# Performance work log

Hardware: AMD Instinct MI355X
Metric: run time of the kernel (lower is better)

## Reference

```python
import jax, jax.numpy as jnp
import numpy as np
import math

B, N, F = 4, 4096, 64
NEG_SLOPE = 0.01


def _leaky_relu(x):
    return jnp.where(x >= 0, x, NEG_SLOPE * x)


def setup_inputs() -> dict:
    key = jax.random.key(0)
    k1, k2, k3, k4, k5 = jax.random.split(key, 5)
    Q = jax.random.normal(k1, (B, N, F, 2), dtype=jnp.float32)
    K = jax.random.normal(k2, (B, N, F, 2), dtype=jnp.float32)
    V = jax.random.normal(k3, (B, N, F, 2), dtype=jnp.float32)
    W_att = jax.random.normal(k4, (F, F), dtype=jnp.float32) / math.sqrt(F)
    b_att = jax.random.normal(k5, (F,), dtype=jnp.float32) * 0.01
    return {"Q": Q, "K": K, "V": V, "W_att": W_att, "b_att": b_att}


def reference(Q, K, V, W_att, b_att):
    # Split complex components: last axis is (real, imag)
    Qr, Qi = Q[..., 0], Q[..., 1]
    Kr, Ki = K[..., 0], K[..., 1]
    Vr, Vi = V[..., 0], V[..., 1]

    n = Q.shape[1]
    scale = 1.0 / math.sqrt(n)  # num_nodes == N

    # Complex scores = Q @ K^T (no conjugation, as in torch einsum on complex)
    sr = (jnp.einsum('bik,bjk->bij', Qr, Kr) - jnp.einsum('bik,bjk->bij', Qi, Ki)) * scale
    si = (jnp.einsum('bik,bjk->bij', Qr, Ki) + jnp.einsum('bik,bjk->bij', Qi, Kr)) * scale

    # Causal mask: positions j > i are masked out (contribute zero weight)
    causal = jnp.tril(jnp.ones((n, n), dtype=bool))  # [N, N], True = keep
    wr = jnp.where(causal, _leaky_relu(sr), 0.0)
    wi = jnp.where(causal, _leaky_relu(si), 0.0)

    # Attention-weighted values (real weights with real V, imag with imag V)
    out_r = jnp.einsum('bij,bjf->bif', wr, Vr)
    out_i = jnp.einsum('bij,bjf->bif', wi, Vi)

    # att_map: shared linear layer
    out_r = out_r @ W_att.T + b_att
    out_i = out_i @ W_att.T + b_att

    return jnp.stack([out_r, out_i], axis=-1)  # [B, N, F, 2]
```

## Files before the change

### kernel.cpp

```cpp
#include <hip/hip_runtime.h>

#define NB 4
#define NN 4096
#define NF 64
#define TSTEP 8
#define BLKS_PER_B 260

typedef __attribute__((ext_vector_type(8))) short bf16x8;
typedef __attribute__((ext_vector_type(4))) float f32x4;

union S8 { unsigned short u[8]; bf16x8 v; };

__device__ __forceinline__ unsigned short f2bf(float x) {
    unsigned int uu = __builtin_bit_cast(unsigned int, x);
    uu += 0x7fffu + ((uu >> 16) & 1u);
    return (unsigned short)(uu >> 16);
}

__global__ __launch_bounds__(256)
void prep_all(const float* __restrict__ Q, const float* __restrict__ K,
              const float* __restrict__ V, const float* __restrict__ W,
              const float* __restrict__ batt,
              short* __restrict__ QF, short* __restrict__ KF,
              short* __restrict__ VF, short* __restrict__ WF,
              float* __restrict__ out) {
    int tid = blockIdx.x * 256 + threadIdx.x;

    if (tid < 262144) {
        int sel = tid >> 17;
        int r   = tid & 0x1FFFF;
        int l  = r & 63;
        int c  = (r >> 6) & 1;
        int rg = (r >> 7) & 255;
        int b  = r >> 15;
        const float* src = sel ? K : Q;
        short*       dst = sel ? KF : QF;
        float sc = sel ? 1.0f : 0.015625f;

        int row = rg * 16 + (l & 15);
        int k0  = c * 32 + (l >> 4) * 8;
        const float4* s4 = (const float4*)src;
        int base4 = (b * NN + row) * 32 + (k0 >> 1);

        S8 ar, ai;
        #pragma unroll
        for (int m = 0; m < 4; ++m) {
            float4 f = s4[base4 + m];
            ar.u[2 * m]     = f2bf(f.x * sc);
            ar.u[2 * m + 1] = f2bf(f.z * sc);
            ai.u[2 * m]     = f2bf(f.y * sc);
            ai.u[2 * m + 1] = f2bf(f.w * sc);
        }
        int cid0 = ((b * 256 + rg) * 2 + c) * 2;
        *(bf16x8*)(dst + (cid0 + 0) * 512 + l * 8) = ar.v;
        *(bf16x8*)(dst + (cid0 + 1) * 512 + l * 8) = ai.v;
    } else if (tid < 393216) {
        int r = tid - 262144;
        int l  = r & 63;
        int c  = (r >> 6) & 1;
        int ft = (r >> 7) & 3;
        int jt = (r >> 9) & 63;
        int b  = (r >> 15) & 3;

        int f  = ft * 16 + (l & 15);
        int jb = jt * 64 + c * 32 + (l >> 4) * 4;
        const float2* s2 = (const float2*)V;

        S8 ar, ai;
        #pragma unroll
        for (int e = 0; e < 8; ++e) {
            int j = jb + (e >> 2) * 16 + (e & 3);
            float2 gg = s2[(b * NN + j) * 64 + f];
            ar.u[e] = f2bf(gg.x);
            ai.u[e] = f2bf(gg.y);
        }
        int cid0 = (((b * 64 + jt) * 4 + ft) * 2 + c) * 2;
        *(bf16x8*)(VF + (cid0 + 0) * 512 + l * 8) = ar.v;
        *(bf16x8*)(VF + (cid0 + 1) * 512 + l * 8) = ai.v;
    } else if (tid < 393728) {
        int r = tid - 393216;
        int l  = r & 63;
        int c  = (r >> 6) & 1;
        int gt = r >> 7;
        int grow = gt * 16 + (l & 15);
        const float* sp = W + grow * 64;
        S8 a;
        #pragma unroll
        for (int e = 0; e < 8; ++e) {
            int f = c * 32 + (e >> 2) * 16 + (l >> 4) * 4 + (e & 3);
            a.u[e] = f2bf(sp[f]);
        }
        *(bf16x8*)(WF + ((gt * 2 + c) * 64 + l) * 8) = a.v;
    } else {
        int r = tid - 393728;
        int g0 = (2 * r) & 63;
        float b0 = batt[g0];
        float b1 = batt[g0 + 1];
        float4 zz = {b0, b0, b1, b1};
        ((float4*)out)[r] = zz;
    }
}

__device__ __forceinline__ int tri_inv(int g) {
    int it = (int)((__builtin_sqrtf(8.0f * (float)g + 1.0f) - 1.0f) * 0.5f);
    while ((it + 1) * (it + 2) / 2 <= g) ++it;
    while (it * (it + 1) / 2 > g) --it;
    return it;
}

__global__ __launch_bounds__(256, 4)
void attn_main(const short* __restrict__ QF, const short* __restrict__ KF,
               const short* __restrict__ VF, const short* __restrict__ WF,
               const float* __restrict__ batt, float* __restrict__ out) {
    int bid = blockIdx.x;
    int b   = bid / BLKS_PER_B;
    int g   = (bid % BLKS_PER_B) * TSTEP;
    int gend = g + TSTEP;

    int w   = threadIdx.x >> 6;
    int l   = threadIdx.x & 63;
    int r16 = l & 15;
    int lb  = l >> 4;

    const f32x4 z = {0.f, 0.f, 0.f, 0.f};

    while (g < gend) {
        int it   = tri_inv(g);
        int base = it * (it + 1) / 2;
        int jt0  = g - base;
        int cnt  = min(gend - g, it + 1 - jt0);
        int jt1  = jt0 + cnt;

        bf16x8 qf[2][2];
        {
            int rgq = it * 4 + w;
            #pragma unroll
            for (int c = 0; c < 2; ++c)
                #pragma unroll
                for (int ch = 0; ch < 2; ++ch)
                    qf[c][ch] = *(const bf16x8*)(QF + (((b * 256 + rgq) * 2 + c) * 2 + ch) * 512 + l * 8);
        }

        f32x4 o[4][2];
        #pragma unroll
        for (int ft = 0; ft < 4; ++ft) { o[ft][0] = z; o[ft][1] = z; }

        for (int jt = jt0; jt < jt1; ++jt) {
            bool diag = (jt == it);
            bf16x8 pa0r, pa0i, pa1r, pa1i;

            #pragma unroll
            for (int ct = 0; ct < 4; ++ct) {
                bf16x8 kf[2][2];
                int rg = jt * 4 + ct;
                #pragma unroll
                for (int c = 0; c < 2; ++c)
                    #pragma unroll
                    for (int ch = 0; ch < 2; ++ch)
                        kf[c][ch] = *(const bf16x8*)(KF + (((b * 256 + rg) * 2 + c) * 2 + ch) * 512 + l * 8);

                f32x4 t1 = __builtin_amdgcn_mfma_f32_16x16x32_bf16(kf[0][0], qf[0][0], z, 0, 0, 0);
                t1 = __builtin_amdgcn_mfma_f32_16x16x32_bf16(kf[1][0], qf[1][0], t1, 0, 0, 0);
                f32x4 t2 = __builtin_amdgcn_mfma_f32_16x16x32_bf16(kf[0][1], qf[0][1], z, 0, 0, 0);
                t2 = __builtin_amdgcn_mfma_f32_16x16x32_bf16(kf[1][1], qf[1][1], t2, 0, 0, 0);
                f32x4 si = __builtin_amdgcn_mfma_f32_16x16x32_bf16(kf[0][1], qf[0][0], z, 0, 0, 0);
                si = __builtin_amdgcn_mfma_f32_16x16x32_bf16(kf[1][1], qf[1][0], si, 0, 0, 0);
                si = __builtin_amdgcn_mfma_f32_16x16x32_bf16(kf[0][0], qf[0][1], si, 0, 0, 0);
                si = __builtin_amdgcn_mfma_f32_16x16x32_bf16(kf[1][0], qf[1][1], si, 0, 0, 0);

                #pragma unroll
                for (int reg = 0; reg < 4; ++reg) {
                    float sr = t1[reg] - t2[reg];
                    float sv = si[reg];
                    float wr = fmaxf(sr, 0.f) + 0.01f * fminf(sr, 0.f);
                    float wi = fmaxf(sv, 0.f) + 0.01f * fminf(sv, 0.f);
                    if (diag) {
                        int jg = ct * 16 + lb * 4 + reg;
                        int ig = w * 16 + r16;
                        if (jg > ig) { wr = 0.f; wi = 0.f; }
                    }
                    short hr = (short)f2bf(wr);
                    short hi = (short)f2bf(wi);
                    int e = (ct & 1) * 4 + reg;
                    if (ct < 2) { pa0r[e] = hr; pa0i[e] = hi; }
                    else        { pa1r[e] = hr; pa1i[e] = hi; }
                }
            }

            #pragma unroll
            for (int ft = 0; ft < 4; ++ft) {
                int cid0 = (((b * 64 + jt) * 4 + ft) * 2 + 0) * 2;
                bf16x8 v0r = *(const bf16x8*)(VF + (cid0 + 0) * 512 + l * 8);
                bf16x8 v0i = *(const bf16x8*)(VF + (cid0 + 1) * 512 + l * 8);
                bf16x8 v1r = *(const bf16x8*)(VF + (cid0 + 2) * 512 + l * 8);
                bf16x8 v1i = *(const bf16x8*)(VF + (cid0 + 3) * 512 + l * 8);
                o[ft][0] = __builtin_amdgcn_mfma_f32_16x16x32_bf16(v0r, pa0r, o[ft][0], 0, 0, 0);
                o[ft][0] = __builtin_amdgcn_mfma_f32_16x16x32_bf16(v1r, pa1r, o[ft][0], 0, 0, 0);
                o[ft][1] = __builtin_amdgcn_mfma_f32_16x16x32_bf16(v0i, pa0i, o[ft][1], 0, 0, 0);
                o[ft][1] = __builtin_amdgcn_mfma_f32_16x16x32_bf16(v1i, pa1i, o[ft][1], 0, 0, 0);
            }
        }

        bf16x8 ob[2][2];
        #pragma unroll
        for (int cc = 0; cc < 2; ++cc)
            #pragma unroll
            for (int ch = 0; ch < 2; ++ch)
                #pragma unroll
                for (int s = 0; s < 2; ++s)
                    #pragma unroll
                    for (int reg = 0; reg < 4; ++reg)
                        ob[cc][ch][s * 4 + reg] = (short)f2bf(o[cc * 2 + s][ch][reg]);

        bool whole = (jt0 == 0) && (jt1 == it + 1);
        int i0 = it * 64 + w * 16;

        #pragma unroll
        for (int gt = 0; gt < 4; ++gt) {
            bf16x8 wa0 = *(const bf16x8*)(WF + ((gt * 2 + 0) * 64 + l) * 8);
            bf16x8 wa1 = *(const bf16x8*)(WF + ((gt * 2 + 1) * 64 + l) * 8);

            f32x4 a0 = __builtin_amdgcn_mfma_f32_16x16x32_bf16(ob[0][0], wa0, z, 0, 0, 0);
            a0 = __builtin_amdgcn_mfma_f32_16x16x32_bf16(ob[1][0], wa1, a0, 0, 0, 0);
            f32x4 a1 = __builtin_amdgcn_mfma_f32_16x16x32_bf16(ob[0][1], wa0, z, 0, 0, 0);
            a1 = __builtin_amdgcn_mfma_f32_16x16x32_bf16(ob[1][1], wa1, a1, 0, 0, 0);

            int gcol = gt * 16 + r16;
            if (whole) {
                float bb = batt[gcol];
                #pragma unroll
                for (int reg = 0; reg < 4; ++reg) {
                    int irow = i0 + lb * 4 + reg;
                    float2 st = {a0[reg] + bb, a1[reg] + bb};
                    *(float2*)(out + ((b * NN + irow) * 64 + gcol) * 2) = st;
                }
            } else {
                #pragma unroll
                for (int reg = 0; reg < 4; ++reg) {
                    int irow = i0 + lb * 4 + reg;
                    int idx = ((b * NN + irow) * 64 + gcol) * 2;
                    atomicAdd(out + idx,     a0[reg]);
                    atomicAdd(out + idx + 1, a1[reg]);
                }
            }
        }

        g += cnt;
    }
}

extern "C" void kernel_launch(void* const* d_in, const int* in_sizes, int n_in,
                              void* d_out, int out_size, void* d_ws, size_t ws_size,
                              hipStream_t stream) {
    const float* Q  = (const float*)d_in[0];
    const float* K  = (const float*)d_in[1];
    const float* V  = (const float*)d_in[2];
    const float* W  = (const float*)d_in[3];
    const float* bA = (const float*)d_in[4];
    float* out = (float*)d_out;

    short* QF = (short*)d_ws;
    short* KF = QF + 2097152;
    short* VF = KF + 2097152;
    short* WF = VF + 2097152;

    prep_all<<<3586, 256, 0, stream>>>(Q, K, V, W, bA, QF, KF, VF, WF, out);
    attn_main<<<NB * BLKS_PER_B, 256, 0, stream>>>(QF, KF, VF, WF, bA, out);
}
```

Baseline: 185.7 us.

## Stage K/V tiles in shared memory and specialize diagonal tile compute

Before this change each of the four waves loaded the full K and V tiles from global memory on its own. Now the block cooperatively loads them once per key tile into a 32 KB LDS buffer, with a barrier before and after, so global/L2 traffic drops about fourfold. The diagonal-mask branch becomes a template parameter so off-diagonal tiles skip the mask check. The hand-written bf16 rounding and leaky-relu are swapped for library and select-based forms. The costs are two barriers per tile with no double buffering, so load latency is no longer overlapped, and more LDS use that may limit occupancy.

```diff
diff --git a/kernel.cpp b/kernel.cpp
--- a/kernel.cpp
+++ b/kernel.cpp
@@ -1,4 +1,5 @@
 #include <hip/hip_runtime.h>
+#include <hip/hip_bf16.h>
 
 #define NB 4
 #define NN 4096
@@ -15,6 +16,10 @@
     unsigned int uu = __builtin_bit_cast(unsigned int, x);
     uu += 0x7fffu + ((uu >> 16) & 1u);
     return (unsigned short)(uu >> 16);
+}
+
+__device__ __forceinline__ short f2bf_s(float x) {
+    return __builtin_bit_cast(short, __float2bfloat16(x));
 }
 
 __global__ __launch_bounds__(256)
@@ -108,10 +113,70 @@
     return it;
 }
 
+template<bool DIAG>
+__device__ __forceinline__ void tile_compute(const short* sb, int w, int l,
+                                             int r16, int lb,
+                                             const bf16x8 (&qf)[2][2],
+                                             f32x4 (&o)[4][2]) {
+    const f32x4 z = {0.f, 0.f, 0.f, 0.f};
+    bf16x8 pa0r, pa0i, pa1r, pa1i;
+
+    #pragma unroll
+    for (int ct = 0; ct < 4; ++ct) {
+        const short* kb = sb + (ct * 4) * 512 + l * 8;
+        bf16x8 kf00 = *(const bf16x8*)(kb);
+        bf16x8 kf01 = *(const bf16x8*)(kb + 512);
+        bf16x8 kf10 = *(const bf16x8*)(kb + 1024);
+        bf16x8 kf11 = *(const bf16x8*)(kb + 1536);
+
+        f32x4 t1 = __builtin_amdgcn_mfma_f32_16x16x32_bf16(kf00, qf[0][0], z, 0, 0, 0);
+        t1 = __builtin_amdgcn_mfma_f32_16x16x32_bf16(kf10, qf[1][0], t1, 0, 0, 0);
+        f32x4 t2 = __builtin_amdgcn_mfma_f32_16x16x32_bf16(kf01, qf[0][1], z, 0, 0, 0);
+        t2 = __builtin_amdgcn_mfma_f32_16x16x32_bf16(kf11, qf[1][1], t2, 0, 0, 0);
+        f32x4 si = __builtin_amdgcn_mfma_f32_16x16x32_bf16(kf01, qf[0][0], z, 0, 0, 0);
+        si = __builtin_amdgcn_mfma_f32_16x16x32_bf16(kf11, qf[1][0], si, 0, 0, 0);
+        si = __builtin_amdgcn_mfma_f32_16x16x32_bf16(kf00, qf[0][1], si, 0, 0, 0);
+        si = __builtin_amdgcn_mfma_f32_16x16x32_bf16(kf10, qf[1][1], si, 0, 0, 0);
+
+        #pragma unroll
+        for (int reg = 0; reg < 4; ++reg) {
+            float sr = t1[reg] - t2[reg];
+            float sv = si[reg];
+            float wr = sr * (sr >= 0.f ? 1.0f : 0.01f);
+            float wi = sv * (sv >= 0.f ? 1.0f : 0.01f);
+            if constexpr (DIAG) {
+                int jg = ct * 16 + lb * 4 + reg;
+                int ig = w * 16 + r16;
+                if (jg > ig) { wr = 0.f; wi = 0.f; }
+            }
+            short hr = f2bf_s(wr);
+            short hi = f2bf_s(wi);
+            int e = (ct & 1) * 4 + reg;
+            if (ct < 2) { pa0r[e] = hr; pa0i[e] = hi; }
+            else        { pa1r[e] = hr; pa1i[e] = hi; }
+        }
+    }
+
+    #pragma unroll
+    for (int ft = 0; ft < 4; ++ft) {
+        const short* vb = sb + (16 + ft * 4) * 512 + l * 8;
+        bf16x8 v0r = *(const bf16x8*)(vb);
+        bf16x8 v0i = *(const bf16x8*)(vb + 512);
+        bf16x8 v1r = *(const bf16x8*)(vb + 1024);
+        bf16x8 v1i = *(const bf16x8*)(vb + 1536);
+        o[ft][0] = __builtin_amdgcn_mfma_f32_16x16x32_bf16(v0r, pa0r, o[ft][0], 0, 0, 0);
+        o[ft][0] = __builtin_amdgcn_mfma_f32_16x16x32_bf16(v1r, pa1r, o[ft][0], 0, 0, 0);
+        o[ft][1] = __builtin_amdgcn_mfma_f32_16x16x32_bf16(v0i, pa0i, o[ft][1], 0, 0, 0);
+        o[ft][1] = __builtin_amdgcn_mfma_f32_16x16x32_bf16(v1i, pa1i, o[ft][1], 0, 0, 0);
+    }
+}
+
 __global__ __launch_bounds__(256, 4)
 void attn_main(const short* __restrict__ QF, const short* __restrict__ KF,
                const short* __restrict__ VF, const short* __restrict__ WF,
                const float* __restrict__ batt, float* __restrict__ out) {
+    __shared__ __align__(16) short sbuf[16384];
+
     int bid = blockIdx.x;
     int b   = bid / BLKS_PER_B;
     int g   = (bid % BLKS_PER_B) * TSTEP;
@@ -146,59 +211,21 @@
         for (int ft = 0; ft < 4; ++ft) { o[ft][0] = z; o[ft][1] = z; }
 
         for (int jt = jt0; jt < jt1; ++jt) {
-            bool diag = (jt == it);
-            bf16x8 pa0r, pa0i, pa1r, pa1i;
-
-            #pragma unroll
-            for (int ct = 0; ct < 4; ++ct) {
-                bf16x8 kf[2][2];
-                int rg = jt * 4 + ct;
-                #pragma unroll
-                for (int c = 0; c < 2; ++c)
-                    #pragma unroll
-                    for (int ch = 0; ch < 2; ++ch)
-                        kf[c][ch] = *(const bf16x8*)(KF + (((b * 256 + rg) * 2 + c) * 2 + ch) * 512 + l * 8);
-
-                f32x4 t1 = __builtin_amdgcn_mfma_f32_16x16x32_bf16(kf[0][0], qf[0][0], z, 0, 0, 0);
-                t1 = __builtin_amdgcn_mfma_f32_16x16x32_bf16(kf[1][0], qf[1][0], t1, 0, 0, 0);
-                f32x4 t2 = __builtin_amdgcn_mfma_f32_16x16x32_bf16(kf[0][1], qf[0][1], z, 0, 0, 0);
-                t2 = __builtin_amdgcn_mfma_f32_16x16x32_bf16(kf[1][1], qf[1][1], t2, 0, 0, 0);
-                f32x4 si = __builtin_amdgcn_mfma_f32_16x16x32_bf16(kf[0][1], qf[0][0], z, 0, 0, 0);
-                si = __builtin_amdgcn_mfma_f32_16x16x32_bf16(kf[1][1], qf[1][0], si, 0, 0, 0);
-                si = __builtin_amdgcn_mfma_f32_16x16x32_bf16(kf[0][0], qf[0][1], si, 0, 0, 0);
-                si = __builtin_amdgcn_mfma_f32_16x16x32_bf16(kf[1][0], qf[1][1], si, 0, 0, 0);
-
-                #pragma unroll
-                for (int reg = 0; reg < 4; ++reg) {
-                    float sr = t1[reg] - t2[reg];
-                    float sv = si[reg];
-                    float wr = fmaxf(sr, 0.f) + 0.01f * fminf(sr, 0.f);
-                    float wi = fmaxf(sv, 0.f) + 0.01f * fminf(sv, 0.f);
-                    if (diag) {
-                        int jg = ct * 16 + lb * 4 + reg;
-                        int ig = w * 16 + r16;
-                        if (jg > ig) { wr = 0.f; wi = 0.f; }
-                    }
-                    short hr = (short)f2bf(wr);
-                    short hi = (short)f2bf(wi);
-                    int e = (ct & 1) * 4 + reg;
-                    if (ct < 2) { pa0r[e] = hr; pa0i[e] = hi; }
-                    else        { pa1r[e] = hr; pa1i[e] = hi; }
+            __syncthreads();
+            {
+                int tb = b * 1024 + jt * 16;
+                #pragma unroll
+                for (int q = 0; q < 8; ++q) {
+                    int c = w * 8 + q;
+                    const short* src = (c < 16)
+                        ? (KF + (tb + c) * 512 + l * 8)
+                        : (VF + (tb + (c - 16)) * 512 + l * 8);
+                    *(bf16x8*)(sbuf + c * 512 + l * 8) = *(const bf16x8*)src;
                 }
             }
-
-            #pragma unroll
-            for (int ft = 0; ft < 4; ++ft) {
-                int cid0 = (((b * 64 + jt) * 4 + ft) * 2 + 0) * 2;
-                bf16x8 v0r = *(const bf16x8*)(VF + (cid0 + 0) * 512 + l * 8);
-                bf16x8 v0i = *(const bf16x8*)(VF + (cid0 + 1) * 512 + l * 8);
-                bf16x8 v1r = *(const bf16x8*)(VF + (cid0 + 2) * 512 + l * 8);
-                bf16x8 v1i = *(const bf16x8*)(VF + (cid0 + 3) * 512 + l * 8);
-                o[ft][0] = __builtin_amdgcn_mfma_f32_16x16x32_bf16(v0r, pa0r, o[ft][0], 0, 0, 0);
-                o[ft][0] = __builtin_amdgcn_mfma_f32_16x16x32_bf16(v1r, pa1r, o[ft][0], 0, 0, 0);
-                o[ft][1] = __builtin_amdgcn_mfma_f32_16x16x32_bf16(v0i, pa0i, o[ft][1], 0, 0, 0);
-                o[ft][1] = __builtin_amdgcn_mfma_f32_16x16x32_bf16(v1i, pa1i, o[ft][1], 0, 0, 0);
-            }
+            __syncthreads();
+            if (jt == it) tile_compute<true >(sbuf, w, l, r16, lb, qf, o);
+            else          tile_compute<false>(sbuf, w, l, r16, lb, qf, o);
         }
 
         bf16x8 ob[2][2];
@@ -210,7 +237,7 @@
                 for (int s = 0; s < 2; ++s)
                     #pragma unroll
                     for (int reg = 0; reg < 4; ++reg)
-                        ob[cc][ch][s * 4 + reg] = (short)f2bf(o[cc * 2 + s][ch][reg]);
+                        ob[cc][ch][s * 4 + reg] = f2bf_s(o[cc * 2 + s][ch][reg]);
 
         bool whole = (jt0 == 0) && (jt1 == it + 1);
         int i0 = it * 64 + w * 16;
```

Result: slower. 268.9 us (+44.9%).
